# Kernel optimization log

Measured on AMD Instinct MI355X. Metric: run time of the kernel, lower is better.

## Reference

```python
import jax, jax.numpy as jnp
import numpy as np

NUM_HEAD = 2
KR = 3          # kernel_range = [3, 3]
SHIFT = 1
N_P = KR * KR   # 9 taps
PAD = (KR // 2) * SHIFT  # 1
OFFSETS = [(i, j) for i in (-(KR // 2), 0, KR // 2) if True for j in ()]  # placeholder, real list below
OFFSETS = [(i, j) for i in range(-(KR // 2), KR // 2 + 1) for j in range(-(KR // 2), KR // 2 + 1)]


def _conv3x3(x, w, b):
    # x: [B,H,W,Cin], w: [3,3,Cin,Cout] -> SAME conv + bias
    y = jax.lax.conv_general_dilated(
        x, w, window_strides=(1, 1), padding='SAME',
        dimension_numbers=('NHWC', 'HWIO', 'NHWC'))
    return y + b


def setup_inputs() -> dict:
    key = jax.random.key(0)
    B, H, W, D = 4, 128, 128, 64
    ks = jax.random.split(key, 10)
    sc = 0.05  # small init like glorot
    return {
        'x': jax.random.normal(ks[0], (B, H, W, D), jnp.float32),
        # 1x1 conv kernels stored as matrices (equiv. to (1,1,Cin,Cout))
        'K_P': jax.random.normal(ks[1], (D, D * N_P), jnp.float32) * sc,
        'V_P': jax.random.normal(ks[2], (D, D * N_P), jnp.float32) * sc,
        'Q_P': jax.random.normal(ks[3], (D, D), jnp.float32) * sc,
        'ff1_kernel': jax.random.normal(ks[4], (D, D), jnp.float32) * sc,
        'ff1_bias': jax.random.normal(ks[5], (D,), jnp.float32) * sc,
        'ff2_kernel': jax.random.normal(ks[6], (3, 3, D, 2 * D), jnp.float32) * sc,
        'ff2_bias': jax.random.normal(ks[7], (2 * D,), jnp.float32) * sc,
        'ff3_kernel': jax.random.normal(ks[8], (3, 3, 2 * D, D), jnp.float32) * sc,
        'ff3_bias': jax.random.normal(ks[9], (D,), jnp.float32) * sc,
    }


def reference(x, K_P, V_P, Q_P, ff1_kernel, ff1_bias, ff2_kernel, ff2_bias,
              ff3_kernel, ff3_bias):
    B, H, W, D = x.shape
    hd = D // NUM_HEAD

    # 1x1 projections; K/V produce N_P channel chunks, one per tap
    x_k = jnp.einsum('bhwd,de->bhwe', x, K_P).reshape(B, H, W, N_P, D)
    x_v = jnp.einsum('bhwd,de->bhwe', x, V_P).reshape(B, H, W, N_P, D)
    x_q = jnp.einsum('bhwd,de->bhwe', x, Q_P)

    pad5 = ((0, 0), (PAD, PAD), (PAD, PAD), (0, 0), (0, 0))
    k_pad = jnp.pad(x_k, pad5)
    v_pad = jnp.pad(x_v, pad5)

    # tap t uses channel chunk t at spatial offset OFFSETS[t]*SHIFT
    def taps(padded):
        return jnp.stack(
            [padded[:, PAD + i * SHIFT:PAD + i * SHIFT + H,
                    PAD + j * SHIFT:PAD + j * SHIFT + W, t, :]
             for t, (i, j) in enumerate(OFFSETS)], axis=3)  # [B,H,W,N_P,D]

    k_taps = taps(k_pad)
    v_taps = taps(v_pad)

    # validity mask (padded taps get score 0 before softmax, as in original)
    m_pad = jnp.pad(jnp.ones((B, H, W), x.dtype), ((0, 0), (PAD, PAD), (PAD, PAD)))
    mask = jnp.stack(
        [m_pad[:, PAD + i * SHIFT:PAD + i * SHIFT + H,
               PAD + j * SHIFT:PAD + j * SHIFT + W]
         for (i, j) in OFFSETS], axis=3)  # [B,H,W,N_P]

    kh = k_taps.reshape(B, H, W, N_P, NUM_HEAD, hd)
    vh = v_taps.reshape(B, H, W, N_P, NUM_HEAD, hd)
    qh = x_q.reshape(B, H, W, NUM_HEAD, hd)

    # scores per head over taps; masked-multiply then /3, as in original
    scores = jnp.einsum('bhwtnc,bhwnc->bhwnt', kh, qh)
    scores = scores * mask[:, :, :, None, :] / 3.0
    alpha = jax.nn.softmax(scores, axis=-1)  # over taps
    attn = jnp.einsum('bhwnt,bhwtnc->bhwnc', alpha, vh).reshape(B, H, W, D)

    # FFN: 1x1 conv -> relu -> 3x3 conv -> relu -> 3x3 conv -> relu
    t = jax.nn.relu(jnp.einsum('bhwd,de->bhwe', attn, ff1_kernel) + ff1_bias)
    t = jax.nn.relu(_conv3x3(t, ff2_kernel, ff2_bias))
    t = jax.nn.relu(_conv3x3(t, ff3_kernel, ff3_bias))
    return t
```

## Files before the change

### kernel.cpp

```cpp
#include <hip/hip_runtime.h>


typedef _Float16 half8 __attribute__((ext_vector_type(8)));
typedef float f32x4 __attribute__((ext_vector_type(4)));

#define PLANE 524288

__device__ __forceinline__ f32x4 mfma16(half8 a, half8 b, f32x4 c) {
  return __builtin_amdgcn_mfma_f32_16x16x32_f16(a, b, c, 0, 0, 0);
}
__device__ __forceinline__ half8 ldfrag(const _Float16* p) { return *(const half8*)p; }
__device__ __forceinline__ half8 zfrag() { half8 z = {}; return z; }

__device__ __forceinline__ void gload_lds16(const _Float16* g, _Float16* l) {
  __builtin_amdgcn_global_load_lds(
      (const __attribute__((address_space(1))) void*)g,
      (__attribute__((address_space(3))) void*)l, 16, 0, 0);
}

__global__ __launch_bounds__(256) void prep(
    const float* __restrict__ x, const float* __restrict__ Kp,
    const float* __restrict__ Vp, const float* __restrict__ Qp,
    const float* __restrict__ W1, const float* __restrict__ F2,
    const float* __restrict__ F3, _Float16* __restrict__ xh,
    _Float16* __restrict__ out) {
  if (blockIdx.x < 2048) {
    const int t = threadIdx.x;
    const int px = blockIdx.x * 32 + (t >> 3);
    const int oct = t & 7;
    const float4* s = (const float4*)(x + (size_t)px * 64 + oct * 8);
    float4 a = s[0], b = s[1];
    half8 h = { (_Float16)a.x, (_Float16)a.y, (_Float16)a.z, (_Float16)a.w,
                (_Float16)b.x, (_Float16)b.y, (_Float16)b.z, (_Float16)b.w };
    *(half8*)(xh + (size_t)oct * PLANE + (size_t)px * 8) = h;
    return;
  }
  int e = (blockIdx.x - 2048) * 256 + threadIdx.x;
  int j = e & 7, l = (e >> 3) & 63, f = e >> 9;
  int l15 = l & 15, q8 = (l >> 4) * 8;
  float v;
  if (f < 8)        { int mb = f >> 1, kb = f & 1;
                      v = Qp[(kb*32 + q8 + j) * 64 + mb*16 + l15]; }
  else if (f < 80)  { int g = f - 8, t = g >> 3, mb = (g >> 1) & 3, kb = g & 1;
                      v = Kp[(kb*32 + q8 + j) * 576 + t*64 + mb*16 + l15]; }
  else if (f < 152) { int g = f - 80, t = g >> 3, kb = (g >> 2) & 1, nb = g & 3;
                      v = Vp[(kb*32 + q8 + j) * 576 + t*64 + nb*16 + l15]; }
  else if (f < 160) { int g = f - 152, kb = g >> 2, nb = g & 3;
                      v = W1[(kb*32 + q8 + j) * 64 + nb*16 + l15]; }
  else if (f < 304) { int g = f - 160, t = g >> 4, kb = (g >> 3) & 1, nb = g & 7;
                      v = F2[(t*64 + kb*32 + q8 + j) * 128 + nb*16 + l15]; }
  else              { int g = f - 304, t = g >> 4, kb = (g >> 2) & 3, nb = g & 3;
                      v = F3[(t*128 + kb*32 + q8 + j) * 64 + nb*16 + l15]; }
  out[e] = (_Float16)v;
}

__global__ __launch_bounds__(512) void attn_ff1(
    const _Float16* __restrict__ xh, const _Float16* __restrict__ wf,
    const float* __restrict__ f1b, _Float16* __restrict__ t1g) {
  extern __shared__ _Float16 smem[];
  const int lane = threadIdx.x & 63, wid = threadIdx.x >> 6;
  const int l15 = lane & 15, q8 = (lane >> 4) * 8;
  const int row = blockIdx.x * 2 + (wid >> 2);
  const int rw = wid & 3;
  const int p0 = row * 128 + rw * 32;
  const int h = row & 127;
  const int w0 = rw * 32;
  const int oct0 = lane >> 4;
  float* dent = (float*)(smem + 77824) + wid * 64;

  {
    const _Float16* gw = wf + 4096 + (size_t)(wid * 19) * 512;
    _Float16* lw = smem + wid * 19 * 512;
    for (int i = 0; i < 19; ++i)
      gload_lds16(gw + i * 512 + lane * 8, lw + i * 512);
  }

  half8 ax0[2], ax1[2];
#pragma unroll
  for (int m = 0; m < 2; ++m) {
    const size_t px = (size_t)(p0 + m * 16 + l15);
    ax0[m] = ldfrag(xh + (size_t)oct0 * PLANE + px * 8);
    ax1[m] = ldfrag(xh + (size_t)(oct0 + 4) * PLANE + px * 8);
  }
  f32x4 qT[2][4];
#pragma unroll
  for (int cb = 0; cb < 4; ++cb) {
    half8 aq0 = ldfrag(wf + (cb * 2 + 0) * 512 + lane * 8);
    half8 aq1 = ldfrag(wf + (cb * 2 + 1) * 512 + lane * 8);
#pragma unroll
    for (int m = 0; m < 2; ++m) {
      f32x4 c = {};
      c = mfma16(aq0, ax0[m], c);
      c = mfma16(aq1, ax1[m], c);
      qT[m][cb] = c;
    }
  }

  auto load_tap = [&](int t, half8 (&x0)[2], half8 (&x1)[2]) {
    const int dh = t / 3 - 1, dw = t % 3 - 1;
    const bool rk = (unsigned)(h + dh) < 128u;
#pragma unroll
    for (int m = 0; m < 2; ++m) {
      const bool cv = rk && ((unsigned)(w0 + m * 16 + l15 + dw) < 128u);
      const size_t px = (size_t)(p0 + m * 16 + l15 + dh * 128 + dw);
      x0[m] = cv ? ldfrag(xh + (size_t)oct0 * PLANE + px * 8) : zfrag();
      x1[m] = cv ? ldfrag(xh + (size_t)(oct0 + 4) * PLANE + px * 8) : zfrag();
    }
  };

  float den0[2] = {0.f, 0.f}, den1[2] = {0.f, 0.f};
  auto score_tap = [&](int t, half8 (&x0)[2], half8 (&x1)[2],
                       float (&e0)[2], float (&e1)[2]) {
    const int dh = t / 3 - 1;
    const bool rowok = (unsigned)(h + dh) < 128u;
    half8 kf[8];
    if (rowok) {
#pragma unroll
      for (int f = 0; f < 8; ++f)
        kf[f] = ldfrag(smem + (t * 8 + f) * 512 + lane * 8);
    }
#pragma unroll
    for (int m = 0; m < 2; ++m) {
      float pa = 0.f, pb = 0.f;
      if (rowok) {
#pragma unroll
        for (int cb = 0; cb < 4; ++cb) {
          f32x4 c = {};
          c = mfma16(kf[cb * 2 + 0], x0[m], c);
          c = mfma16(kf[cb * 2 + 1], x1[m], c);
          float d = qT[m][cb].x * c.x + qT[m][cb].y * c.y
                  + qT[m][cb].z * c.z + qT[m][cb].w * c.w;
          if (cb < 2) pa += d; else pb += d;
        }
        pa += __shfl_xor(pa, 16, 64); pa += __shfl_xor(pa, 32, 64);
        pb += __shfl_xor(pb, 16, 64); pb += __shfl_xor(pb, 32, 64);
      }
      e0[m] = __expf(pa * (1.f / 3.f));
      e1[m] = __expf(pb * (1.f / 3.f));
      den0[m] += e0[m]; den1[m] += e1[m];
    }
  };

  half8 q0[5][2], q1[5][2];
  load_tap(0, q0[0], q1[0]);
  load_tap(1, q0[1], q1[1]);
  load_tap(2, q0[2], q1[2]);
  load_tap(3, q0[3], q1[3]);

  __syncthreads();

  float e0c[2], e1c[2];
  score_tap(0, q0[0], q1[0], e0c, e1c);

  const _Float16* BVl = smem + 36864;
  f32x4 at[2][4];
#pragma unroll
  for (int m = 0; m < 2; ++m)
#pragma unroll
    for (int nb = 0; nb < 4; ++nb) at[m][nb] = f32x4{};

#pragma unroll
  for (int t = 0; t < 9; ++t) {
    if (t + 4 < 9) load_tap(t + 4, q0[(t + 4) % 5], q1[(t + 4) % 5]);
    const bool rowok = (unsigned)(h + (t / 3 - 1)) < 128u;
    if (rowok) {
      half8 vf[8];
#pragma unroll
      for (int f = 0; f < 8; ++f) vf[f] = ldfrag(BVl + (t * 8 + f) * 512 + lane * 8);
#pragma unroll
      for (int m = 0; m < 2; ++m) {
        _Float16 h0 = (_Float16)e0c[m], h1 = (_Float16)e1c[m];
        half8 b0 = {h0, h0, h0, h0, h0, h0, h0, h0};
        half8 b1 = {h1, h1, h1, h1, h1, h1, h1, h1};
        half8 s00 = q0[t % 5][m] * b0, s01 = q1[t % 5][m] * b0;
        half8 s10 = q0[t % 5][m] * b1, s11 = q1[t % 5][m] * b1;
#pragma unroll
        for (int nb = 0; nb < 2; ++nb) {
          at[m][nb]     = mfma16(s00, vf[0 * 4 + nb],     at[m][nb]);
          at[m][nb]     = mfma16(s01, vf[1 * 4 + nb],     at[m][nb]);
          at[m][nb + 2] = mfma16(s10, vf[0 * 4 + nb + 2], at[m][nb + 2]);
          at[m][nb + 2] = mfma16(s11, vf[1 * 4 + nb + 2], at[m][nb + 2]);
        }
      }
    }
    if (t < 8) {
      float e0n[2], e1n[2];
      score_tap(t + 1, q0[(t + 1) % 5], q1[(t + 1) % 5], e0n, e1n);
#pragma unroll
      for (int m = 0; m < 2; ++m) { e0c[m] = e0n[m]; e1c[m] = e1n[m]; }
    }
  }

#pragma unroll
  for (int m = 0; m < 2; ++m) {
    dent[(m * 2 + 0) * 16 + l15] = den0[m];
    dent[(m * 2 + 1) * 16 + l15] = den1[m];
  }
  f32x4 iv[2][2];
#pragma unroll
  for (int m = 0; m < 2; ++m)
#pragma unroll
    for (int hd = 0; hd < 2; ++hd) {
      f32x4 dv = *(const f32x4*)(dent + (m * 2 + hd) * 16 + (lane >> 4) * 4);
      iv[m][hd] = f32x4{1.f / dv.x, 1.f / dv.y, 1.f / dv.z, 1.f / dv.w};
    }

  __syncthreads();
  _Float16* myt = smem + wid * 2304;
#pragma unroll
  for (int m = 0; m < 2; ++m)
#pragma unroll
    for (int nb = 0; nb < 4; ++nb) {
      const int hd = nb >> 1;
#pragma unroll
      for (int r = 0; r < 4; ++r)
        myt[m * 1152 + ((lane >> 4) * 4 + r) * 72 + nb * 16 + l15] =
            (_Float16)(at[m][nb][r] * iv[m][hd][r]);
    }
  const _Float16* B1l = smem + 73728;
  const int pxl = lane >> 2;
  const int co0 = lane & 3;
#pragma unroll
  for (int m = 0; m < 2; ++m) {
    _Float16* T = myt + m * 1152;
    half8 aa0 = ldfrag(T + l15 * 72 + q8);
    half8 aa1 = ldfrag(T + l15 * 72 + 32 + q8);
#pragma unroll
    for (int nb = 0; nb < 4; ++nb) {
      f32x4 c = {};
      c = mfma16(aa0, ldfrag(B1l + (0 * 4 + nb) * 512 + lane * 8), c);
      c = mfma16(aa1, ldfrag(B1l + (1 * 4 + nb) * 512 + lane * 8), c);
      float bv = f1b[nb * 16 + l15];
#pragma unroll
      for (int r = 0; r < 4; ++r)
        T[((lane >> 4) * 4 + r) * 72 + nb * 16 + l15] =
            (_Float16)fmaxf(c[r] + bv, 0.f);
    }
    const size_t pxg = (size_t)(p0 + m * 16 + pxl);
    half8 h0 = ldfrag(T + pxl * 72 + co0 * 8);
    half8 h1 = ldfrag(T + pxl * 72 + (co0 + 4) * 8);
    *(half8*)(t1g + (size_t)co0 * PLANE + pxg * 8) = h0;
    *(half8*)(t1g + (size_t)(co0 + 4) * PLANE + pxg * 8) = h1;
  }
}

template <int KB, int NBL, int COUT, int DEPTH>
__global__ __launch_bounds__(512, 4) void conv3x3(
    const _Float16* __restrict__ in, const _Float16* __restrict__ wfrag,
    const float* __restrict__ bias, void* __restrict__ outp, int out_fp32) {
  extern __shared__ _Float16 smem[];
  constexpr int NS = DEPTH + 1;
  const int lane = threadIdx.x & 63, wid = threadIdx.x >> 6;
  const int l15 = lane & 15;
  const int nh = blockIdx.x & 1;
  const int pairIdx = blockIdx.x >> 1;
  const int row = pairIdx * 2 + (wid >> 2);
  const int rw = wid & 3;
  const int p0 = row * 128 + rw * 32;
  const int h = row & 127;
  const int w0 = rw * 32;
  const int NBF = COUT / 16;
  const int oct0 = lane >> 4;

  {
    for (int s = 0; s < 9; ++s) {
      int f = wid * 9 + s;
      int t = f >> 3, r = f & 7, kb = r / NBL, i = r % NBL;
      const _Float16* g = wfrag + (size_t)((t * KB + kb) * NBF + nh * NBL + i) * 512;
      gload_lds16(g + lane * 8, smem + f * 512);
    }
  }

  f32x4 acc[2][NBL];
#pragma unroll
  for (int m = 0; m < 2; ++m)
#pragma unroll
    for (int nb = 0; nb < NBL; ++nb) acc[m][nb] = f32x4{};

  auto load_conv = [&](int t, half8 (&dst)[2][KB]) {
    const int dh = t / 3 - 1, dw = t % 3 - 1;
    const bool rk = (unsigned)(h + dh) < 128u;
#pragma unroll
    for (int m = 0; m < 2; ++m) {
      const bool cv = rk && ((unsigned)(w0 + m * 16 + l15 + dw) < 128u);
      const size_t px = (size_t)(p0 + m * 16 + l15 + dh * 128 + dw);
#pragma unroll
      for (int kb = 0; kb < KB; ++kb)
        dst[m][kb] = cv ? ldfrag(in + (size_t)(kb * 4 + oct0) * PLANE + px * 8) : zfrag();
    }
  };

  half8 aq[NS][2][KB];
#pragma unroll
  for (int d = 0; d < DEPTH; ++d) load_conv(d, aq[d]);

  __syncthreads();

#pragma unroll
  for (int t = 0; t < 9; ++t) {
    if (t + DEPTH < 9) load_conv(t + DEPTH, aq[(t + DEPTH) % NS]);
    const bool rowok = (unsigned)(h + (t / 3 - 1)) < 128u;
    if (rowok) {
#pragma unroll
      for (int nb = 0; nb < NBL; ++nb) {
#pragma unroll
        for (int kb = 0; kb < KB; ++kb) {
          half8 b = ldfrag(smem + (size_t)((t * KB + kb) * NBL + nb) * 512 + lane * 8);
          acc[0][nb] = mfma16(aq[t % NS][0][kb], b, acc[0][nb]);
          acc[1][nb] = mfma16(aq[t % NS][1][kb], b, acc[1][nb]);
        }
      }
    }
  }

  if (out_fp32) {
#pragma unroll
    for (int m = 0; m < 2; ++m)
#pragma unroll
      for (int nb = 0; nb < NBL; ++nb) {
        const int ch = nh * NBL * 16 + nb * 16 + l15;
        float bv = bias[ch];
#pragma unroll
        for (int r = 0; r < 4; ++r) {
          float v = fmaxf(acc[m][nb][r] + bv, 0.f);
          size_t px = (size_t)(p0 + m * 16 + (lane >> 4) * 4 + r);
          ((float*)outp)[px * COUT + ch] = v;
        }
      }
  } else {
    __syncthreads();
    _Float16* T = smem + wid * 1152;
    const int pxl = lane >> 2, co0 = lane & 3;
#pragma unroll
    for (int m = 0; m < 2; ++m) {
#pragma unroll
      for (int nb = 0; nb < NBL; ++nb) {
        const int chl = nb * 16 + l15;
        float bv = bias[nh * NBL * 16 + chl];
#pragma unroll
        for (int r = 0; r < 4; ++r)
          T[((lane >> 4) * 4 + r) * 72 + chl] =
              (_Float16)fmaxf(acc[m][nb][r] + bv, 0.f);
      }
      const size_t pxg = (size_t)(p0 + m * 16 + pxl);
      half8 h0 = ldfrag(T + pxl * 72 + co0 * 8);
      half8 h1 = ldfrag(T + pxl * 72 + (co0 + 4) * 8);
      *(half8*)((_Float16*)outp + (size_t)(nh * 8 + co0) * PLANE + pxg * 8) = h0;
      *(half8*)((_Float16*)outp + (size_t)(nh * 8 + co0 + 4) * PLANE + pxg * 8) = h1;
    }
  }
}

__global__ __launch_bounds__(512, 4) void conv3b(
    const _Float16* __restrict__ in, const _Float16* __restrict__ wfrag,
    const float* __restrict__ bias, float* __restrict__ outp) {
  extern __shared__ _Float16 smem[];
  const int lane = threadIdx.x & 63, wid = threadIdx.x >> 6;
  const int l15 = lane & 15;
  const int nh = blockIdx.x & 1;
  const int pairIdx = blockIdx.x >> 1;
  const int row = pairIdx * 2 + (wid >> 2);
  const int rw = wid & 3;
  const int p0 = row * 128 + rw * 32;
  const int h = row & 127;
  const int w0 = rw * 32;
  const int oct0 = lane >> 4;
  const int KB = 4, NBL = 2, NBF = 4, COUT = 64;

  {
    for (int s = 0; s < 9; ++s) {
      int f = wid * 9 + s;
      int t = f >> 3, r = f & 7, kb = r / NBL, i = r % NBL;
      const _Float16* g = wfrag + (size_t)((t * KB + kb) * NBF + nh * NBL + i) * 512;
      gload_lds16(g + lane * 8, smem + f * 512);
    }
  }

  f32x4 acc[2][2];
#pragma unroll
  for (int m = 0; m < 2; ++m)
#pragma unroll
    for (int nb = 0; nb < 2; ++nb) acc[m][nb] = f32x4{};

#pragma unroll
  for (int p = 0; p < 2; ++p) {
    auto load_half = [&](int t, half8 (&dst)[2][2]) {
      const int dh = t / 3 - 1, dw = t % 3 - 1;
      const bool rk = (unsigned)(h + dh) < 128u;
#pragma unroll
      for (int m = 0; m < 2; ++m) {
        const bool cv = rk && ((unsigned)(w0 + m * 16 + l15 + dw) < 128u);
        const size_t px = (size_t)(p0 + m * 16 + l15 + dh * 128 + dw);
#pragma unroll
        for (int kbl = 0; kbl < 2; ++kbl)
          dst[m][kbl] = cv
              ? ldfrag(in + (size_t)((2 * p + kbl) * 4 + oct0) * PLANE + px * 8)
              : zfrag();
      }
    };

    half8 aq[3][2][2];
    load_half(0, aq[0]);
    load_half(1, aq[1]);
    if (p == 0) __syncthreads();

#pragma unroll
    for (int t = 0; t < 9; ++t) {
      if (t + 2 < 9) load_half(t + 2, aq[(t + 2) % 3]);
      const bool rowok = (unsigned)(h + (t / 3 - 1)) < 128u;
      if (rowok) {
#pragma unroll
        for (int nb = 0; nb < 2; ++nb) {
#pragma unroll
          for (int kbl = 0; kbl < 2; ++kbl) {
            half8 b = ldfrag(smem +
                (size_t)((t * KB + 2 * p + kbl) * NBL + nb) * 512 + lane * 8);
            acc[0][nb] = mfma16(aq[t % 3][0][kbl], b, acc[0][nb]);
            acc[1][nb] = mfma16(aq[t % 3][1][kbl], b, acc[1][nb]);
          }
        }
      }
    }
  }

#pragma unroll
  for (int m = 0; m < 2; ++m)
#pragma unroll
    for (int nb = 0; nb < 2; ++nb) {
      const int ch = nh * 32 + nb * 16 + l15;
      float bv = bias[ch];
#pragma unroll
      for (int r = 0; r < 4; ++r) {
        float v = fmaxf(acc[m][nb][r] + bv, 0.f);
        size_t px = (size_t)(p0 + m * 16 + (lane >> 4) * 4 + r);
        outp[px * COUT + ch] = v;
      }
    }
}

extern "C" void kernel_launch(void* const* d_in, const int* in_sizes, int n_in,
                              void* d_out, int out_size, void* d_ws, size_t ws_size,
                              hipStream_t stream) {
  (void)in_sizes; (void)n_in; (void)out_size; (void)ws_size;
  const float* x   = (const float*)d_in[0];
  const float* Kp  = (const float*)d_in[1];
  const float* Vp  = (const float*)d_in[2];
  const float* Qp  = (const float*)d_in[3];
  const float* f1w = (const float*)d_in[4];
  const float* f1b = (const float*)d_in[5];
  const float* f2w = (const float*)d_in[6];
  const float* f2b = (const float*)d_in[7];
  const float* f3w = (const float*)d_in[8];
  const float* f3b = (const float*)d_in[9];

  _Float16* xh  = (_Float16*)d_ws;
  _Float16* wf  = xh + 4194304;
  _Float16* t1g = wf + 229376;
  _Float16* t2g = t1g + 4194304;
  float* outp = (float*)d_out;

  (void)hipFuncSetAttribute((const void*)attn_ff1,
      hipFuncAttributeMaxDynamicSharedMemorySize, 157696);
  (void)hipFuncSetAttribute((const void*)conv3x3<2, 4, 128, 3>,
      hipFuncAttributeMaxDynamicSharedMemorySize, 73728);
  (void)hipFuncSetAttribute((const void*)conv3b,
      hipFuncAttributeMaxDynamicSharedMemorySize, 73728);

  prep<<<2944, 256, 0, stream>>>(x, Kp, Vp, Qp, f1w, f2w, f3w, xh, wf);
  attn_ff1<<<256, 512, 157696, stream>>>(xh, wf, f1b, t1g);
  conv3x3<2, 4, 128, 3><<<512, 512, 73728, stream>>>(t1g, wf + 81920, f2b, t2g, 0);
  conv3b<<<512, 512, 73728, stream>>>(t2g, wf + 155648, f3b, outp);
}
```

Before: 138.4 us.

## Split attention block into 16 waves of 16 pixels each

The attention+ff1 kernel now launches 1024 threads per block instead of 512. Each wave handles 16 pixels instead of 32, which drops the per-wave m-loop and halves accumulator and prefetch register state. Tap prefetch depth falls from 4 to 2, and the LDS weight staging is redistributed across 16 waves. The goal is more resident waves per CU to hide memory latency, since LDS usage already limits each CU to one block. The risk is that the (1024, 4) launch bound forces a tight VGPR budget and causes spills, and the shallower prefetch may expose more load latency.

```diff
diff --git a/kernel.cpp b/kernel.cpp
--- a/kernel.cpp
+++ b/kernel.cpp
@@ -54,63 +54,57 @@
   out[e] = (_Float16)v;
 }
 
-__global__ __launch_bounds__(512) void attn_ff1(
+__global__ __launch_bounds__(1024, 4) void attn_ff1(
     const _Float16* __restrict__ xh, const _Float16* __restrict__ wf,
     const float* __restrict__ f1b, _Float16* __restrict__ t1g) {
   extern __shared__ _Float16 smem[];
   const int lane = threadIdx.x & 63, wid = threadIdx.x >> 6;
   const int l15 = lane & 15, q8 = (lane >> 4) * 8;
-  const int row = blockIdx.x * 2 + (wid >> 2);
-  const int rw = wid & 3;
-  const int p0 = row * 128 + rw * 32;
+  const int row = blockIdx.x * 2 + (wid >> 3);
+  const int rw = wid & 7;
+  const int p0 = row * 128 + rw * 16;
   const int h = row & 127;
-  const int w0 = rw * 32;
+  const int w0 = rw * 16;
   const int oct0 = lane >> 4;
-  float* dent = (float*)(smem + 77824) + wid * 64;
+  float* dent = (float*)(smem + 77824) + wid * 32;
 
   {
-    const _Float16* gw = wf + 4096 + (size_t)(wid * 19) * 512;
-    _Float16* lw = smem + wid * 19 * 512;
-    for (int i = 0; i < 19; ++i)
-      gload_lds16(gw + i * 512 + lane * 8, lw + i * 512);
-  }
-
-  half8 ax0[2], ax1[2];
-#pragma unroll
-  for (int m = 0; m < 2; ++m) {
-    const size_t px = (size_t)(p0 + m * 16 + l15);
-    ax0[m] = ldfrag(xh + (size_t)oct0 * PLANE + px * 8);
-    ax1[m] = ldfrag(xh + (size_t)(oct0 + 4) * PLANE + px * 8);
-  }
-  f32x4 qT[2][4];
+    for (int i = 0; i < 10; ++i) {
+      int f = wid * 10 + i;
+      if (f < 152)
+        gload_lds16(wf + 4096 + (size_t)f * 512 + lane * 8,
+                    smem + (size_t)f * 512);
+    }
+  }
+
+  half8 ax0, ax1;
+  {
+    const size_t px = (size_t)(p0 + l15);
+    ax0 = ldfrag(xh + (size_t)oct0 * PLANE + px * 8);
+    ax1 = ldfrag(xh + (size_t)(oct0 + 4) * PLANE + px * 8);
+  }
+  f32x4 qT[4];
 #pragma unroll
   for (int cb = 0; cb < 4; ++cb) {
     half8 aq0 = ldfrag(wf + (cb * 2 + 0) * 512 + lane * 8);
     half8 aq1 = ldfrag(wf + (cb * 2 + 1) * 512 + lane * 8);
-#pragma unroll
-    for (int m = 0; m < 2; ++m) {
-      f32x4 c = {};
-      c = mfma16(aq0, ax0[m], c);
-      c = mfma16(aq1, ax1[m], c);
-      qT[m][cb] = c;
-    }
-  }
-
-  auto load_tap = [&](int t, half8 (&x0)[2], half8 (&x1)[2]) {
+    f32x4 c = {};
+    c = mfma16(aq0, ax0, c);
+    c = mfma16(aq1, ax1, c);
+    qT[cb] = c;
+  }
+
+  auto load_tap = [&](int t, half8& x0, half8& x1) {
     const int dh = t / 3 - 1, dw = t % 3 - 1;
     const bool rk = (unsigned)(h + dh) < 128u;
-#pragma unroll
-    for (int m = 0; m < 2; ++m) {
-      const bool cv = rk && ((unsigned)(w0 + m * 16 + l15 + dw) < 128u);
-      const size_t px = (size_t)(p0 + m * 16 + l15 + dh * 128 + dw);
-      x0[m] = cv ? ldfrag(xh + (size_t)oct0 * PLANE + px * 8) : zfrag();
-      x1[m] = cv ? ldfrag(xh + (size_t)(oct0 + 4) * PLANE + px * 8) : zfrag();
-    }
+    const bool cv = rk && ((unsigned)(w0 + l15 + dw) < 128u);
+    const size_t px = (size_t)(p0 + l15 + dh * 128 + dw);
+    x0 = cv ? ldfrag(xh + (size_t)oct0 * PLANE + px * 8) : zfrag();
+    x1 = cv ? ldfrag(xh + (size_t)(oct0 + 4) * PLANE + px * 8) : zfrag();
   };
 
-  float den0[2] = {0.f, 0.f}, den1[2] = {0.f, 0.f};
-  auto score_tap = [&](int t, half8 (&x0)[2], half8 (&x1)[2],
-                       float (&e0)[2], float (&e1)[2]) {
+  float den0 = 0.f, den1 = 0.f;
+  auto score_tap = [&](int t, half8& x0, half8& x1, float& e0, float& e1) {
     const int dh = t / 3 - 1;
     const bool rowok = (unsigned)(h + dh) < 128u;
     half8 kf[8];
@@ -119,129 +113,108 @@
       for (int f = 0; f < 8; ++f)
         kf[f] = ldfrag(smem + (t * 8 + f) * 512 + lane * 8);
     }
-#pragma unroll
-    for (int m = 0; m < 2; ++m) {
-      float pa = 0.f, pb = 0.f;
-      if (rowok) {
-#pragma unroll
-        for (int cb = 0; cb < 4; ++cb) {
-          f32x4 c = {};
-          c = mfma16(kf[cb * 2 + 0], x0[m], c);
-          c = mfma16(kf[cb * 2 + 1], x1[m], c);
-          float d = qT[m][cb].x * c.x + qT[m][cb].y * c.y
-                  + qT[m][cb].z * c.z + qT[m][cb].w * c.w;
-          if (cb < 2) pa += d; else pb += d;
-        }
-        pa += __shfl_xor(pa, 16, 64); pa += __shfl_xor(pa, 32, 64);
-        pb += __shfl_xor(pb, 16, 64); pb += __shfl_xor(pb, 32, 64);
-      }
-      e0[m] = __expf(pa * (1.f / 3.f));
-      e1[m] = __expf(pb * (1.f / 3.f));
-      den0[m] += e0[m]; den1[m] += e1[m];
-    }
+    float pa = 0.f, pb = 0.f;
+    if (rowok) {
+#pragma unroll
+      for (int cb = 0; cb < 4; ++cb) {
+        f32x4 c = {};
+        c = mfma16(kf[cb * 2 + 0], x0, c);
+        c = mfma16(kf[cb * 2 + 1], x1, c);
+        float d = qT[cb].x * c.x + qT[cb].y * c.y
+                + qT[cb].z * c.z + qT[cb].w * c.w;
+        if (cb < 2) pa += d; else pb += d;
+      }
+      pa += __shfl_xor(pa, 16, 64); pa += __shfl_xor(pa, 32, 64);
+      pb += __shfl_xor(pb, 16, 64); pb += __shfl_xor(pb, 32, 64);
+    }
+    e0 = __expf(pa * (1.f / 3.f));
+    e1 = __expf(pb * (1.f / 3.f));
+    den0 += e0; den1 += e1;
   };
 
-  half8 q0[5][2], q1[5][2];
+  half8 q0[3], q1[3];
   load_tap(0, q0[0], q1[0]);
   load_tap(1, q0[1], q1[1]);
-  load_tap(2, q0[2], q1[2]);
-  load_tap(3, q0[3], q1[3]);
 
   __syncthreads();
 
-  float e0c[2], e1c[2];
+  float e0c, e1c;
   score_tap(0, q0[0], q1[0], e0c, e1c);
 
   const _Float16* BVl = smem + 36864;
-  f32x4 at[2][4];
-#pragma unroll
-  for (int m = 0; m < 2; ++m)
-#pragma unroll
-    for (int nb = 0; nb < 4; ++nb) at[m][nb] = f32x4{};
+  f32x4 at[4];
+#pragma unroll
+  for (int nb = 0; nb < 4; ++nb) at[nb] = f32x4{};
 
 #pragma unroll
   for (int t = 0; t < 9; ++t) {
-    if (t + 4 < 9) load_tap(t + 4, q0[(t + 4) % 5], q1[(t + 4) % 5]);
+    if (t + 2 < 9) load_tap(t + 2, q0[(t + 2) % 3], q1[(t + 2) % 3]);
     const bool rowok = (unsigned)(h + (t / 3 - 1)) < 128u;
     if (rowok) {
       half8 vf[8];
 #pragma unroll
-      for (int f = 0; f < 8; ++f) vf[f] = ldfrag(BVl + (t * 8 + f) * 512 + lane * 8);
-#pragma unroll
-      for (int m = 0; m < 2; ++m) {
-        _Float16 h0 = (_Float16)e0c[m], h1 = (_Float16)e1c[m];
-        half8 b0 = {h0, h0, h0, h0, h0, h0, h0, h0};
-        half8 b1 = {h1, h1, h1, h1, h1, h1, h1, h1};
-        half8 s00 = q0[t % 5][m] * b0, s01 = q1[t % 5][m] * b0;
-        half8 s10 = q0[t % 5][m] * b1, s11 = q1[t % 5][m] * b1;
-#pragma unroll
-        for (int nb = 0; nb < 2; ++nb) {
-          at[m][nb]     = mfma16(s00, vf[0 * 4 + nb],     at[m][nb]);
-          at[m][nb]     = mfma16(s01, vf[1 * 4 + nb],     at[m][nb]);
-          at[m][nb + 2] = mfma16(s10, vf[0 * 4 + nb + 2], at[m][nb + 2]);
-          at[m][nb + 2] = mfma16(s11, vf[1 * 4 + nb + 2], at[m][nb + 2]);
-        }
+      for (int f = 0; f < 8; ++f)
+        vf[f] = ldfrag(BVl + (t * 8 + f) * 512 + lane * 8);
+      _Float16 h0 = (_Float16)e0c, h1 = (_Float16)e1c;
+      half8 b0 = {h0, h0, h0, h0, h0, h0, h0, h0};
+      half8 b1 = {h1, h1, h1, h1, h1, h1, h1, h1};
+      half8 s00 = q0[t % 3] * b0, s01 = q1[t % 3] * b0;
+      half8 s10 = q0[t % 3] * b1, s11 = q1[t % 3] * b1;
+#pragma unroll
+      for (int nb = 0; nb < 2; ++nb) {
+        at[nb]     = mfma16(s00, vf[0 * 4 + nb],     at[nb]);
+        at[nb]     = mfma16(s01, vf[1 * 4 + nb],     at[nb]);
+        at[nb + 2] = mfma16(s10, vf[0 * 4 + nb + 2], at[nb + 2]);
+        at[nb + 2] = mfma16(s11, vf[1 * 4 + nb + 2], at[nb + 2]);
       }
     }
     if (t < 8) {
-      float e0n[2], e1n[2];
-      score_tap(t + 1, q0[(t + 1) % 5], q1[(t + 1) % 5], e0n, e1n);
-#pragma unroll
-      for (int m = 0; m < 2; ++m) { e0c[m] = e0n[m]; e1c[m] = e1n[m]; }
-    }
-  }
-
-#pragma unroll
-  for (int m = 0; m < 2; ++m) {
-    dent[(m * 2 + 0) * 16 + l15] = den0[m];
-    dent[(m * 2 + 1) * 16 + l15] = den1[m];
-  }
-  f32x4 iv[2][2];
-#pragma unroll
-  for (int m = 0; m < 2; ++m)
-#pragma unroll
-    for (int hd = 0; hd < 2; ++hd) {
-      f32x4 dv = *(const f32x4*)(dent + (m * 2 + hd) * 16 + (lane >> 4) * 4);
-      iv[m][hd] = f32x4{1.f / dv.x, 1.f / dv.y, 1.f / dv.z, 1.f / dv.w};
-    }
+      float e0n, e1n;
+      score_tap(t + 1, q0[(t + 1) % 3], q1[(t + 1) % 3], e0n, e1n);
+      e0c = e0n; e1c = e1n;
+    }
+  }
+
+  dent[0 * 16 + l15] = den0;
+  dent[1 * 16 + l15] = den1;
+  f32x4 iv[2];
+#pragma unroll
+  for (int hd = 0; hd < 2; ++hd) {
+    f32x4 dv = *(const f32x4*)(dent + hd * 16 + (lane >> 4) * 4);
+    iv[hd] = f32x4{1.f / dv.x, 1.f / dv.y, 1.f / dv.z, 1.f / dv.w};
+  }
 
   __syncthreads();
-  _Float16* myt = smem + wid * 2304;
-#pragma unroll
-  for (int m = 0; m < 2; ++m)
-#pragma unroll
-    for (int nb = 0; nb < 4; ++nb) {
-      const int hd = nb >> 1;
-#pragma unroll
-      for (int r = 0; r < 4; ++r)
-        myt[m * 1152 + ((lane >> 4) * 4 + r) * 72 + nb * 16 + l15] =
-            (_Float16)(at[m][nb][r] * iv[m][hd][r]);
-    }
+  _Float16* myt = smem + wid * 1152;
+#pragma unroll
+  for (int nb = 0; nb < 4; ++nb) {
+    const int hd = nb >> 1;
+#pragma unroll
+    for (int r = 0; r < 4; ++r)
+      myt[((lane >> 4) * 4 + r) * 72 + nb * 16 + l15] =
+          (_Float16)(at[nb][r] * iv[hd][r]);
+  }
   const _Float16* B1l = smem + 73728;
   const int pxl = lane >> 2;
   const int co0 = lane & 3;
-#pragma unroll
-  for (int m = 0; m < 2; ++m) {
-    _Float16* T = myt + m * 1152;
-    half8 aa0 = ldfrag(T + l15 * 72 + q8);
-    half8 aa1 = ldfrag(T + l15 * 72 + 32 + q8);
-#pragma unroll
-    for (int nb = 0; nb < 4; ++nb) {
-      f32x4 c = {};
-      c = mfma16(aa0, ldfrag(B1l + (0 * 4 + nb) * 512 + lane * 8), c);
-      c = mfma16(aa1, ldfrag(B1l + (1 * 4 + nb) * 512 + lane * 8), c);
-      float bv = f1b[nb * 16 + l15];
-#pragma unroll
-      for (int r = 0; r < 4; ++r)
-        T[((lane >> 4) * 4 + r) * 72 + nb * 16 + l15] =
-            (_Float16)fmaxf(c[r] + bv, 0.f);
-    }
-    const size_t pxg = (size_t)(p0 + m * 16 + pxl);
-    half8 h0 = ldfrag(T + pxl * 72 + co0 * 8);
-    half8 h1 = ldfrag(T + pxl * 72 + (co0 + 4) * 8);
-    *(half8*)(t1g + (size_t)co0 * PLANE + pxg * 8) = h0;
-    *(half8*)(t1g + (size_t)(co0 + 4) * PLANE + pxg * 8) = h1;
-  }
+  half8 aa0 = ldfrag(myt + l15 * 72 + q8);
+  half8 aa1 = ldfrag(myt + l15 * 72 + 32 + q8);
+#pragma unroll
+  for (int nb = 0; nb < 4; ++nb) {
+    f32x4 c = {};
+    c = mfma16(aa0, ldfrag(B1l + (0 * 4 + nb) * 512 + lane * 8), c);
+    c = mfma16(aa1, ldfrag(B1l + (1 * 4 + nb) * 512 + lane * 8), c);
+    float bv = f1b[nb * 16 + l15];
+#pragma unroll
+    for (int r = 0; r < 4; ++r)
+      myt[((lane >> 4) * 4 + r) * 72 + nb * 16 + l15] =
+          (_Float16)fmaxf(c[r] + bv, 0.f);
+  }
+  const size_t pxg = (size_t)(p0 + pxl);
+  half8 h0 = ldfrag(myt + pxl * 72 + co0 * 8);
+  half8 h1 = ldfrag(myt + pxl * 72 + (co0 + 4) * 8);
+  *(half8*)(t1g + (size_t)co0 * PLANE + pxg * 8) = h0;
+  *(half8*)(t1g + (size_t)(co0 + 4) * PLANE + pxg * 8) = h1;
 }
 
 template <int KB, int NBL, int COUT, int DEPTH>
@@ -467,7 +440,7 @@
       hipFuncAttributeMaxDynamicSharedMemorySize, 73728);
 
   prep<<<2944, 256, 0, stream>>>(x, Kp, Vp, Qp, f1w, f2w, f3w, xh, wf);
-  attn_ff1<<<256, 512, 157696, stream>>>(xh, wf, f1b, t1g);
+  attn_ff1<<<256, 1024, 157696, stream>>>(xh, wf, f1b, t1g);
   conv3x3<2, 4, 128, 3><<<512, 512, 73728, stream>>>(t1g, wf + 81920, f2b, t2g, 0);
   conv3b<<<512, 512, 73728, stream>>>(t2g, wf + 155648, f3b, outp);
 }
```

Result: no change. 137.7 us (-0.5%).
